# Kernel tuning notes

Hardware: AMD Instinct MI355X
Metric: run time of the kernel (lower is better)

## Reference

```python
import jax, jax.numpy as jnp
import numpy as np

GAMMA = 0.7
WALK_LEN = 3
TAU = 1.0
N_FILTERS = 8


def _row_norm(A):
    return A / jnp.clip(jnp.sum(A, axis=-1, keepdims=True), 1e-12, None)


def _motif_channel(A, idx, Wadj, gates):
    # A: [n,n]; idx: [I,k] int node indices; Wadj: [F,k,k]; gates: [L]
    n = A.shape[0]
    I, k = idx.shape
    F = Wadj.shape[0]
    # learnable filter adjacency: softplus, symmetrize, zero diagonal, row-normalize
    S = jax.nn.softplus(Wadj)
    S = 0.5 * (S + jnp.swapaxes(S, -1, -2)) * (1.0 - jnp.eye(k, dtype=A.dtype))
    Sf = _row_norm(S)                                  # [F,k,k]
    # per-instance induced subgraph transition matrices
    As = A[idx[:, :, None], idx[:, None, :]]           # [I,k,k]
    Tm = _row_norm(As)                                 # [I,k,k]
    # batched Kronecker product: Km[i,f,a*k+b,c*k+d] = Tm[i,a,c]*Sf[f,b,d]
    Km = (Tm[:, None, :, None, :, None] * Sf[None, :, None, :, None, :]).reshape(I, F, k * k, k * k)
    gp = jax.nn.softplus(gates)                        # [L] length gates
    M = Km
    acc = (GAMMA * gp[0]) * jnp.trace(M, axis1=-2, axis2=-1)   # [I,F]
    for p in range(2, WALK_LEN + 1):
        M = M @ Km
        acc = acc + (GAMMA ** p * gp[p - 1]) * jnp.trace(M, axis1=-2, axis2=-1)
    sims = acc                                         # [I,F] RWK similarities
    alphas = jax.nn.softmax(sims / max(1e-06, TAU), axis=-1)
    contrib = (alphas * sims) / float(k)               # [I,F]
    upd = jnp.broadcast_to(contrib[:, None, :], (I, k, F)).reshape(I * k, F)
    return jnp.zeros((n, F), A.dtype).at[idx.reshape(-1)].add(upd)


def _layer(A, tri_idx, cyc_idx, H, Wt, Wc, g, lng, lnb, w1, b1, w2, b2):
    Phi = jnp.concatenate([_motif_channel(A, tri_idx, Wt, g),
                           _motif_channel(A, cyc_idx, Wc, g),
                           H], axis=1)                 # [n, in_ch]
    mu = jnp.mean(Phi, axis=-1, keepdims=True)
    var = jnp.var(Phi, axis=-1, keepdims=True)
    X = (Phi - mu) / jnp.sqrt(var + 1e-5) * lng + lnb  # LayerNorm
    return jax.nn.gelu(X @ w1 + b1, approximate=False) @ w2 + b2  # dropout = identity (eval)


def _templates():
    tri = np.zeros((3, 3), np.float32)
    for u, v in [(0, 1), (1, 2), (0, 2)]:
        tri[u, v] = tri[v, u] = 1.0
    cyc = np.zeros((4, 4), np.float32)
    for u, v in [(0, 1), (1, 2), (2, 3), (3, 0)]:
        cyc[u, v] = cyc[v, u] = 1.0
    return tri, cyc


def setup_inputs() -> dict:
    key = jax.random.key(0)
    ks = jax.random.split(key, 16)
    n, D, HID = 4096, 128, 128
    A = (jax.random.uniform(ks[0], (n, n)) < 0.01).astype(jnp.float32)
    A = 0.5 * (A + A.T)
    A = A * (1.0 - jnp.eye(n, dtype=jnp.float32))
    tri_idx = jax.random.randint(ks[1], (30000, 3), 0, n, dtype=jnp.int32)
    cyc_idx = jax.random.randint(ks[2], (15000, 4), 0, n, dtype=jnp.int32)
    tri_t, cyc_t = _templates()
    def w_adj(k, tmpl):
        return jnp.asarray(tmpl)[None] + 0.05 * jax.random.normal(k, (N_FILTERS,) + tmpl.shape, dtype=jnp.float32)
    in0, in1 = 17, 145
    inp = {"A_full": A, "tri_idx": tri_idx, "cyc_idx": cyc_idx,
           "W_tri_0": w_adj(ks[3], tri_t), "W_cyc_0": w_adj(ks[4], cyc_t),
           "gates_0": jnp.zeros((WALK_LEN,), jnp.float32),
           "lng_0": jnp.ones((in0,), jnp.float32), "lnb_0": jnp.zeros((in0,), jnp.float32),
           "w1_0": 0.05 * jax.random.normal(ks[5], (in0, HID), jnp.float32), "b1_0": jnp.zeros((HID,), jnp.float32),
           "w2_0": 0.05 * jax.random.normal(ks[6], (HID, D), jnp.float32), "b2_0": jnp.zeros((D,), jnp.float32),
           "W_tri_1": w_adj(ks[7], tri_t), "W_cyc_1": w_adj(ks[8], cyc_t),
           "gates_1": jnp.zeros((WALK_LEN,), jnp.float32),
           "lng_1": jnp.ones((in1,), jnp.float32), "lnb_1": jnp.zeros((in1,), jnp.float32),
           "w1_1": 0.05 * jax.random.normal(ks[9], (in1, HID), jnp.float32), "b1_1": jnp.zeros((HID,), jnp.float32),
           "w2_1": 0.05 * jax.random.normal(ks[10], (HID, D), jnp.float32), "b2_1": jnp.zeros((D,), jnp.float32)}
    return inp


def reference(A_full, tri_idx, cyc_idx,
              W_tri_0, W_cyc_0, gates_0, lng_0, lnb_0, w1_0, b1_0, w2_0, b2_0,
              W_tri_1, W_cyc_1, gates_1, lng_1, lnb_1, w1_1, b1_1, w2_1, b2_1):
    # base channel (use_base=True): node degree from dense adjacency
    H = jnp.sum(A_full, axis=-1, keepdims=True)        # [n,1]
    Z = _layer(A_full, tri_idx, cyc_idx, H, W_tri_0, W_cyc_0, gates_0, lng_0, lnb_0, w1_0, b1_0, w2_0, b2_0)
    H = jnp.concatenate([Z, H], axis=1)                # residual_cat: [n,129]
    Z = _layer(A_full, tri_idx, cyc_idx, H, W_tri_1, W_cyc_1, gates_1, lng_1, lnb_1, w1_1, b1_1, w2_1, b2_1)
    H = jnp.concatenate([Z, H], axis=1)                # [n,257]
    return H
```

## Files before the change

kernel.cpp:

```cpp
#include <hip/hip_runtime.h>
#include <math.h>
#include <stdint.h>

#define GAMMA 0.7f
#define CAP 96

typedef __attribute__((ext_vector_type(8))) short short8v;
typedef __attribute__((ext_vector_type(4))) float f32x4;

__device__ __forceinline__ float sp_dev(float x) {
    return fmaxf(x, 0.0f) + log1pf(expf(-fabsf(x)));
}
__device__ __forceinline__ float gelu_exact(float x) {
    return 0.5f * x * (1.0f + erff(x * 0.70710678118654752f));
}
__device__ __forceinline__ uint16_t f2bf(float x) {
    union { float f; uint32_t u; } c; c.f = x;
    uint32_t u = c.u + 0x7FFFu + ((c.u >> 16) & 1u);
    return (uint16_t)(u >> 16);
}

__global__ void prep_kernel(const float* __restrict__ Wt0, const float* __restrict__ Wc0,
                            const float* __restrict__ g0,
                            const float* __restrict__ Wt1, const float* __restrict__ Wc1,
                            const float* __restrict__ g1,
                            const float* __restrict__ w1_0, const float* __restrict__ w2_0,
                            const float* __restrict__ w1_1, const float* __restrict__ w2_1,
                            float* __restrict__ dcoef,
                            uint16_t* __restrict__ Wb10, uint16_t* __restrict__ Wb20,
                            uint16_t* __restrict__ Wb11, uint16_t* __restrict__ Wb21,
                            int* __restrict__ cursor, int ncur) {
    int tid = threadIdx.x;
    int gtid = blockIdx.x * blockDim.x + tid;
    int stride = gridDim.x * blockDim.x;

    for (int i = gtid; i < ncur; i += stride) cursor[i] = 0;

    if (blockIdx.x == 0 && tid < 32) {
        int L = tid >> 4, m = (tid >> 3) & 1, f = tid & 7;
        int k = m ? 4 : 3;
        const float* W = L ? (m ? Wc1 : Wt1) : (m ? Wc0 : Wt0);
        const float* g = L ? g1 : g0;
        float S[4][4], Y[4][4];
        for (int a = 0; a < k; a++)
            for (int b = 0; b < k; b++)
                S[a][b] = sp_dev(W[(f * k + a) * k + b]);
        for (int a = 0; a < k; a++)
            for (int b = 0; b < k; b++)
                Y[a][b] = (a == b) ? 0.0f : 0.5f * (S[a][b] + S[b][a]);
        for (int a = 0; a < k; a++) {
            float rs = 0.0f;
            for (int b = 0; b < k; b++) rs += Y[a][b];
            rs = fmaxf(rs, 1e-12f);
            for (int b = 0; b < k; b++) Y[a][b] /= rs;
        }
        float t1 = 0, t2 = 0, t3 = 0;
        for (int a = 0; a < k; a++) t1 += Y[a][a];
        for (int a = 0; a < k; a++)
            for (int b = 0; b < k; b++) t2 += Y[a][b] * Y[b][a];
        for (int a = 0; a < k; a++)
            for (int b = 0; b < k; b++)
                for (int c = 0; c < k; c++) t3 += Y[a][b] * Y[b][c] * Y[c][a];
        float* d = dcoef + ((L * 2 + m) * 8 + f) * 3;
        d[0] = GAMMA * sp_dev(g[0]) * t1;
        d[1] = GAMMA * GAMMA * sp_dev(g[1]) * t2;
        d[2] = GAMMA * GAMMA * GAMMA * sp_dev(g[2]) * t3;
    }
    for (int idx = gtid; idx < 57344; idx += stride) {
        if (idx < 4096) {
            int c = idx >> 5, k = idx & 31;
            Wb10[idx] = (k < 17) ? f2bf(w1_0[k * 128 + c]) : 0;
        } else if (idx < 20480) {
            int e = idx - 4096; int c = e >> 7, k = e & 127;
            Wb20[e] = f2bf(w2_0[k * 128 + c]);
        } else if (idx < 40960) {
            int e = idx - 20480; int c = e / 160, k = e % 160;
            Wb11[e] = (k < 145) ? f2bf(w1_1[k * 128 + c]) : 0;
        } else {
            int e = idx - 40960; int c = e >> 7, k = e & 127;
            Wb21[e] = f2bf(w2_1[k * 128 + c]);
        }
    }
}

__global__ void rowsum_kernel(const float* __restrict__ A, int n,
                              float* __restrict__ H0, float* __restrict__ out) {
    int row = blockIdx.x;
    const float4* Arow = (const float4*)(A + (size_t)row * n);
    int n4 = n >> 2;
    float s = 0.0f;
    for (int i = threadIdx.x; i < n4; i += blockDim.x) {
        float4 v = Arow[i];
        s += v.x + v.y + v.z + v.w;
    }
    __shared__ float red[4];
    for (int off = 32; off > 0; off >>= 1) s += __shfl_down(s, off);
    if ((threadIdx.x & 63) == 0) red[threadIdx.x >> 6] = s;
    __syncthreads();
    if (threadIdx.x == 0) {
        float t = red[0] + red[1] + red[2] + red[3];
        H0[row] = t;
        out[(size_t)row * 257 + 256] = t;
    }
}

template <int K>
__device__ __forceinline__ void contrib_body(
    const float* __restrict__ A, int n, const int* __restrict__ idx, int I, int i,
    const float (*dc)[8][3], float* __restrict__ cont,
    int* __restrict__ cursor, int* __restrict__ slotbuf) {
    int nodes[K];
#pragma unroll
    for (int j = 0; j < K; j++) nodes[j] = idx[i * K + j];

    float Tm[K][K];
#pragma unroll
    for (int a = 0; a < K; a++) {
        float rs = 0.0f;
#pragma unroll
        for (int b = 0; b < K; b++) {
            float v = A[(size_t)nodes[a] * n + nodes[b]];
            Tm[a][b] = v; rs += v;
        }
        rs = fmaxf(rs, 1e-12f);
        float inv = 1.0f / rs;
#pragma unroll
        for (int b = 0; b < K; b++) Tm[a][b] *= inv;
    }
    float t1 = 0, t2 = 0, t3 = 0;
#pragma unroll
    for (int a = 0; a < K; a++) t1 += Tm[a][a];
#pragma unroll
    for (int a = 0; a < K; a++)
#pragma unroll
        for (int b = 0; b < K; b++) t2 += Tm[a][b] * Tm[b][a];
#pragma unroll
    for (int a = 0; a < K; a++)
#pragma unroll
        for (int b = 0; b < K; b++) {
            float ab = Tm[a][b];
#pragma unroll
            for (int c = 0; c < K; c++) t3 += ab * Tm[b][c] * Tm[c][a];
        }
#pragma unroll
    for (int L = 0; L < 2; L++) {
        float sims[8], mx = -1e30f;
#pragma unroll
        for (int f = 0; f < 8; f++) {
            sims[f] = dc[L][f][0] * t1 + dc[L][f][1] * t2 + dc[L][f][2] * t3;
            mx = fmaxf(mx, sims[f]);
        }
        float es[8], se = 0.0f;
#pragma unroll
        for (int f = 0; f < 8; f++) { es[f] = expf(sims[f] - mx); se += es[f]; }
        float inv = 1.0f / se;
        float* cp = cont + ((size_t)L * I + i) * 8;
#pragma unroll
        for (int f = 0; f < 8; f++) cp[f] = es[f] * inv * sims[f] * (1.0f / (float)K);
    }
#pragma unroll
    for (int j = 0; j < K; j++) {
        int v = nodes[j];
        int pos = atomicAdd(&cursor[v], 1);
        if (pos < CAP) slotbuf[(size_t)v * CAP + pos] = i;
    }
}

__global__ void contrib_fused_kernel(const float* __restrict__ A, int n,
                                     const int* __restrict__ tri, int Itri,
                                     const int* __restrict__ cyc, int Icyc, int B3,
                                     const float* __restrict__ dcoef,
                                     float* __restrict__ tri_c, float* __restrict__ cyc_c,
                                     int* __restrict__ cursor, int* __restrict__ slotbuf) {
    __shared__ float dc[2][8][3];
    int tid = threadIdx.x;
    bool isTri = (int)blockIdx.x < B3;
    const float* dcL0 = dcoef + (isTri ? 0 : 24);
    const float* dcL1 = dcoef + (isTri ? 48 : 72);
    if (tid < 24) dc[0][tid / 3][tid % 3] = dcL0[tid];
    else if (tid < 48) { int t = tid - 24; dc[1][t / 3][t % 3] = dcL1[t]; }
    __syncthreads();

    if (isTri) {
        int i = blockIdx.x * 256 + tid;
        if (i < Itri)
            contrib_body<3>(A, n, tri, Itri, i, dc, tri_c, cursor, slotbuf);
    } else {
        int i = (blockIdx.x - B3) * 256 + tid;
        if (i < Icyc)
            contrib_body<4>(A, n, cyc, Icyc, i, dc, cyc_c, cursor + n,
                            slotbuf + (size_t)n * CAP);
    }
}

__global__ __launch_bounds__(512) void mega_kernel(
    const float* __restrict__ tri_c, int Itri,
    const float* __restrict__ cyc_c, int Icyc,
    const int* __restrict__ cursor, const int* __restrict__ slotbuf,
    const float* __restrict__ H0,
    const float* __restrict__ lng0, const float* __restrict__ lnb0,
    const uint16_t* __restrict__ Wb10, const float* __restrict__ b1_0,
    const uint16_t* __restrict__ Wb20, const float* __restrict__ b2_0,
    const float* __restrict__ lng1, const float* __restrict__ lnb1,
    const uint16_t* __restrict__ Wb11, const float* __restrict__ b1_1,
    const uint16_t* __restrict__ Wb21, const float* __restrict__ b2_1,
    float* __restrict__ out, int n) {
    __shared__ uint16_t Xs[16][168];
    __shared__ uint16_t Hs[16][136];
    __shared__ float    Zs[16][129];
    __shared__ float    phi0[16][17];
    __shared__ float    f1[16][16];
    __shared__ float    h0s[16];

    int tid = threadIdx.x;
    int v0 = blockIdx.x * 16;
    int wave = tid >> 6;
    int lane = tid & 63;
    int lr = lane & 15, lg = lane >> 4;

    {
        int r = tid >> 5;
        int combo = tid & 31;
        int m = combo >> 4, L = (combo >> 3) & 1, f = combo & 7;
        int v = v0 + r;
        int cnt = cursor[m * n + v];
        cnt = cnt < CAP ? cnt : CAP;
        const int* bucket = slotbuf + ((size_t)(m * n + v)) * CAP;
        const float* c = m ? cyc_c : tri_c;
        int I = m ? Icyc : Itri;
        float sum = 0.0f;
        for (int j = 0; j < cnt; j++) {
            int i = bucket[j];
            sum += c[((size_t)L * I + i) * 8 + f];
        }
        if (L == 0) phi0[r][m * 8 + f] = sum;
        else        f1[r][m * 8 + f] = sum;
        if (combo == 0) { float h = H0[v]; phi0[r][16] = h; h0s[r] = h; }
    }
    __syncthreads();

    {
        int r = tid >> 5;
        int j = tid & 31;
        float x = (j < 17) ? phi0[r][j] : 0.0f;
        float s1 = x, s2 = x * x;
        for (int o = 16; o > 0; o >>= 1) { s1 += __shfl_xor(s1, o); s2 += __shfl_xor(s2, o); }
        float mu = s1 / 17.0f;
        float rstd = rsqrtf(s2 / 17.0f - mu * mu + 1e-5f);
        Xs[r][j] = (j < 17) ? f2bf((x - mu) * rstd * lng0[j] + lnb0[j]) : (uint16_t)0;
    }
    __syncthreads();

    {
        int col = wave * 16 + lr;
        f32x4 acc = {0.f, 0.f, 0.f, 0.f};
        short8v a = *(const short8v*)&Xs[lr][lg * 8];
        short8v b = *(const short8v*)(Wb10 + (size_t)col * 32 + lg * 8);
        acc = __builtin_amdgcn_mfma_f32_16x16x32_bf16(a, b, acc, 0, 0, 0);
        float bias = b1_0[col];
#pragma unroll
        for (int i = 0; i < 4; i++)
            Hs[lg * 4 + i][col] = f2bf(gelu_exact(acc[i] + bias));
    }
    __syncthreads();

    {
        int col = wave * 16 + lr;
        f32x4 acc = {0.f, 0.f, 0.f, 0.f};
#pragma unroll
        for (int ks = 0; ks < 4; ks++) {
            short8v a = *(const short8v*)&Hs[lr][ks * 32 + lg * 8];
            short8v b = *(const short8v*)(Wb20 + (size_t)col * 128 + ks * 32 + lg * 8);
            acc = __builtin_amdgcn_mfma_f32_16x16x32_bf16(a, b, acc, 0, 0, 0);
        }
        float bias = b2_0[col];
#pragma unroll
        for (int i = 0; i < 4; i++) {
            int row = lg * 4 + i;
            float val = acc[i] + bias;
            out[(size_t)(v0 + row) * 257 + 128 + col] = val;
            Zs[row][col] = val;
        }
    }
    __syncthreads();

    {
        int rr = tid >> 5;
        int t = tid & 31;
        float ph[5];
        float s1 = 0.0f, s2 = 0.0f;
#pragma unroll
        for (int s = 0; s < 5; s++) {
            int j = t + 32 * s;
            float x = 0.0f;
            if (j < 16) x = f1[rr][j];
            else if (j < 144) x = Zs[rr][j - 16];
            else if (j == 144) x = h0s[rr];
            ph[s] = x;
            if (j < 145) { s1 += x; s2 += x * x; }
        }
        for (int o = 16; o > 0; o >>= 1) { s1 += __shfl_xor(s1, o); s2 += __shfl_xor(s2, o); }
        float mu = s1 / 145.0f;
        float rstd = rsqrtf(s2 / 145.0f - mu * mu + 1e-5f);
#pragma unroll
        for (int s = 0; s < 5; s++) {
            int j = t + 32 * s;
            Xs[rr][j] = (j < 145) ? f2bf((ph[s] - mu) * rstd * lng1[j] + lnb1[j]) : (uint16_t)0;
        }
    }
    __syncthreads();

    {
        int col = wave * 16 + lr;
        f32x4 acc = {0.f, 0.f, 0.f, 0.f};
#pragma unroll
        for (int ks = 0; ks < 5; ks++) {
            short8v a = *(const short8v*)&Xs[lr][ks * 32 + lg * 8];
            short8v b = *(const short8v*)(Wb11 + (size_t)col * 160 + ks * 32 + lg * 8);
            acc = __builtin_amdgcn_mfma_f32_16x16x32_bf16(a, b, acc, 0, 0, 0);
        }
        float bias = b1_1[col];
#pragma unroll
        for (int i = 0; i < 4; i++)
            Hs[lg * 4 + i][col] = f2bf(gelu_exact(acc[i] + bias));
    }
    __syncthreads();

    {
        int col = wave * 16 + lr;
        f32x4 acc = {0.f, 0.f, 0.f, 0.f};
#pragma unroll
        for (int ks = 0; ks < 4; ks++) {
            short8v a = *(const short8v*)&Hs[lr][ks * 32 + lg * 8];
            short8v b = *(const short8v*)(Wb21 + (size_t)col * 128 + ks * 32 + lg * 8);
            acc = __builtin_amdgcn_mfma_f32_16x16x32_bf16(a, b, acc, 0, 0, 0);
        }
        float bias = b2_1[col];
#pragma unroll
        for (int i = 0; i < 4; i++) {
            int row = lg * 4 + i;
            out[(size_t)(v0 + row) * 257 + col] = acc[i] + bias;
        }
    }
}

extern "C" void kernel_launch(void* const* d_in, const int* in_sizes, int n_in,
                              void* d_out, int out_size, void* d_ws, size_t ws_size,
                              hipStream_t stream) {
    const float* A    = (const float*)d_in[0];
    const int*   tri  = (const int*)d_in[1];
    const int*   cyc  = (const int*)d_in[2];
    const float* Wt0  = (const float*)d_in[3];
    const float* Wc0  = (const float*)d_in[4];
    const float* g0   = (const float*)d_in[5];
    const float* lng0 = (const float*)d_in[6];
    const float* lnb0 = (const float*)d_in[7];
    const float* w1_0 = (const float*)d_in[8];
    const float* b1_0 = (const float*)d_in[9];
    const float* w2_0 = (const float*)d_in[10];
    const float* b2_0 = (const float*)d_in[11];
    const float* Wt1  = (const float*)d_in[12];
    const float* Wc1  = (const float*)d_in[13];
    const float* g1   = (const float*)d_in[14];
    const float* lng1 = (const float*)d_in[15];
    const float* lnb1 = (const float*)d_in[16];
    const float* w1_1 = (const float*)d_in[17];
    const float* b1_1 = (const float*)d_in[18];
    const float* w2_1 = (const float*)d_in[19];
    const float* b2_1 = (const float*)d_in[20];

    int n    = out_size / 257;
    int Itri = in_sizes[1] / 3;
    int Icyc = in_sizes[2] / 4;

    float* ws    = (float*)d_ws;
    float* dcoef = ws;
    float* H0    = ws + 128;
    float* tri_c = H0 + n;
    float* cyc_c = tri_c + (size_t)2 * Itri * 8;
    int*   cursor  = (int*)(cyc_c + (size_t)2 * Icyc * 8);
    int*   slotbuf = cursor + (size_t)2 * n;
    uint16_t* Wb10 = (uint16_t*)(slotbuf + (size_t)2 * n * CAP);
    uint16_t* Wb20 = Wb10 + 128 * 32;
    uint16_t* Wb11 = Wb20 + 128 * 128;
    uint16_t* Wb21 = Wb11 + 128 * 160;
    float* out = (float*)d_out;

    prep_kernel<<<64, 256, 0, stream>>>(Wt0, Wc0, g0, Wt1, Wc1, g1,
                                        w1_0, w2_0, w1_1, w2_1,
                                        dcoef, Wb10, Wb20, Wb11, Wb21,
                                        cursor, 2 * n);

    rowsum_kernel<<<n, 256, 0, stream>>>(A, n, H0, out);

    int B3 = (Itri + 255) / 256;
    int B4 = (Icyc + 255) / 256;
    contrib_fused_kernel<<<B3 + B4, 256, 0, stream>>>(
        A, n, tri, Itri, cyc, Icyc, B3, dcoef, tri_c, cyc_c, cursor, slotbuf);

    mega_kernel<<<n / 16, 512, 0, stream>>>(
        tri_c, Itri, cyc_c, Icyc, cursor, slotbuf, H0,
        lng0, lnb0, Wb10, b1_0, Wb20, b2_0,
        lng1, lnb1, Wb11, b1_1, Wb21, b2_1, out, n);
}
```

Before: 77.05 us.

## Fuse all stages into one kernel with per-block instance scanning

Replaces the four-kernel pipeline (prep, rowsum, contrib, mega) with a single kernel per 16-node tile. Each block recomputes the filter coefficients, sums its own adjacency rows, scans every triangle and cycle instance to queue those touching its nodes, recomputes their similarities and accumulates them with shared-memory atomics, then reads weights directly from fp32 with on-the-fly bf16 conversion. This removes three launches and the global slot buckets and cursor atomics. In exchange every block rereads the whole instance list and recomputes contributions for shared instances, and the MLP weight fragments are converted redundantly in every block.

Result: slower. 90.93 us (+18.0%).

```diff
diff --git a/kernel.cpp b/kernel.cpp
--- a/kernel.cpp
+++ b/kernel.cpp
@@ -3,7 +3,8 @@
 #include <stdint.h>
 
 #define GAMMA 0.7f
-#define CAP 96
+#define QCAP 4608
+#define NT 1024
 
 typedef __attribute__((ext_vector_type(8))) short short8v;
 typedef __attribute__((ext_vector_type(4))) float f32x4;
@@ -20,23 +21,49 @@
     return (uint16_t)(u >> 16);
 }
 
-__global__ void prep_kernel(const float* __restrict__ Wt0, const float* __restrict__ Wc0,
-                            const float* __restrict__ g0,
-                            const float* __restrict__ Wt1, const float* __restrict__ Wc1,
-                            const float* __restrict__ g1,
-                            const float* __restrict__ w1_0, const float* __restrict__ w2_0,
-                            const float* __restrict__ w1_1, const float* __restrict__ w2_1,
-                            float* __restrict__ dcoef,
-                            uint16_t* __restrict__ Wb10, uint16_t* __restrict__ Wb20,
-                            uint16_t* __restrict__ Wb11, uint16_t* __restrict__ Wb21,
-                            int* __restrict__ cursor, int ncur) {
-    int tid = threadIdx.x;
-    int gtid = blockIdx.x * blockDim.x + tid;
-    int stride = gridDim.x * blockDim.x;
-
-    for (int i = gtid; i < ncur; i += stride) cursor[i] = 0;
-
-    if (blockIdx.x == 0 && tid < 32) {
+__device__ __forceinline__ short8v wfrag(const float* __restrict__ W, int col,
+                                         int k0, int kmax) {
+    short8v r;
+#pragma unroll
+    for (int j = 0; j < 8; j++) {
+        int k = k0 + j;
+        float v = (k < kmax) ? W[(size_t)k * 128 + col] : 0.0f;
+        r[j] = (short)f2bf(v);
+    }
+    return r;
+}
+
+__global__ __launch_bounds__(NT) void uber_kernel(
+    const float* __restrict__ A, const int* __restrict__ tri, const int* __restrict__ cyc,
+    const float* __restrict__ Wt0, const float* __restrict__ Wc0, const float* __restrict__ g0,
+    const float* __restrict__ lng0, const float* __restrict__ lnb0,
+    const float* __restrict__ w1_0, const float* __restrict__ b1_0,
+    const float* __restrict__ w2_0, const float* __restrict__ b2_0,
+    const float* __restrict__ Wt1, const float* __restrict__ Wc1, const float* __restrict__ g1,
+    const float* __restrict__ lng1, const float* __restrict__ lnb1,
+    const float* __restrict__ w1_1, const float* __restrict__ b1_1,
+    const float* __restrict__ w2_1, const float* __restrict__ b2_1,
+    float* __restrict__ out, int n, int Itri, int Icyc) {
+
+    __shared__ __align__(16) char upool[QCAP * 4];
+    int* queue = (int*)upool;
+    uint16_t (*Xs)[168] = (uint16_t(*)[168])upool;
+    uint16_t (*Hs)[136] = (uint16_t(*)[136])(upool + 5376);
+    float    (*Zs)[132] = (float(*)[132])(upool + 9728);
+    __shared__ float dcs[2][2][8][3];
+    __shared__ float phiL0[16][16];
+    __shared__ float phiL1[16][16];
+    __shared__ float h0s[16];
+    __shared__ int qcnt;
+
+    const int tid  = threadIdx.x;
+    const int v0   = blockIdx.x * 16;
+    const int wave = tid >> 6;
+    const int lane = tid & 63;
+
+    if (tid < 256) { ((float*)phiL0)[tid] = 0.0f; ((float*)phiL1)[tid] = 0.0f; }
+    if (tid == 0) qcnt = 0;
+    if (tid < 32) {
         int L = tid >> 4, m = (tid >> 3) & 1, f = tid & 7;
         int k = m ? 4 : 3;
         const float* W = L ? (m ? Wc1 : Wt1) : (m ? Wc0 : Wt0);
@@ -61,188 +88,142 @@
         for (int a = 0; a < k; a++)
             for (int b = 0; b < k; b++)
                 for (int c = 0; c < k; c++) t3 += Y[a][b] * Y[b][c] * Y[c][a];
-        float* d = dcoef + ((L * 2 + m) * 8 + f) * 3;
-        d[0] = GAMMA * sp_dev(g[0]) * t1;
-        d[1] = GAMMA * GAMMA * sp_dev(g[1]) * t2;
-        d[2] = GAMMA * GAMMA * GAMMA * sp_dev(g[2]) * t3;
-    }
-    for (int idx = gtid; idx < 57344; idx += stride) {
-        if (idx < 4096) {
-            int c = idx >> 5, k = idx & 31;
-            Wb10[idx] = (k < 17) ? f2bf(w1_0[k * 128 + c]) : 0;
-        } else if (idx < 20480) {
-            int e = idx - 4096; int c = e >> 7, k = e & 127;
-            Wb20[e] = f2bf(w2_0[k * 128 + c]);
-        } else if (idx < 40960) {
-            int e = idx - 20480; int c = e / 160, k = e % 160;
-            Wb11[e] = (k < 145) ? f2bf(w1_1[k * 128 + c]) : 0;
-        } else {
-            int e = idx - 40960; int c = e >> 7, k = e & 127;
-            Wb21[e] = f2bf(w2_1[k * 128 + c]);
-        }
-    }
-}
-
-__global__ void rowsum_kernel(const float* __restrict__ A, int n,
-                              float* __restrict__ H0, float* __restrict__ out) {
-    int row = blockIdx.x;
-    const float4* Arow = (const float4*)(A + (size_t)row * n);
-    int n4 = n >> 2;
-    float s = 0.0f;
-    for (int i = threadIdx.x; i < n4; i += blockDim.x) {
-        float4 v = Arow[i];
-        s += v.x + v.y + v.z + v.w;
-    }
-    __shared__ float red[4];
-    for (int off = 32; off > 0; off >>= 1) s += __shfl_down(s, off);
-    if ((threadIdx.x & 63) == 0) red[threadIdx.x >> 6] = s;
-    __syncthreads();
-    if (threadIdx.x == 0) {
-        float t = red[0] + red[1] + red[2] + red[3];
-        H0[row] = t;
-        out[(size_t)row * 257 + 256] = t;
-    }
-}
-
-template <int K>
-__device__ __forceinline__ void contrib_body(
-    const float* __restrict__ A, int n, const int* __restrict__ idx, int I, int i,
-    const float (*dc)[8][3], float* __restrict__ cont,
-    int* __restrict__ cursor, int* __restrict__ slotbuf) {
-    int nodes[K];
-#pragma unroll
-    for (int j = 0; j < K; j++) nodes[j] = idx[i * K + j];
-
-    float Tm[K][K];
-#pragma unroll
-    for (int a = 0; a < K; a++) {
-        float rs = 0.0f;
-#pragma unroll
-        for (int b = 0; b < K; b++) {
-            float v = A[(size_t)nodes[a] * n + nodes[b]];
-            Tm[a][b] = v; rs += v;
-        }
-        rs = fmaxf(rs, 1e-12f);
-        float inv = 1.0f / rs;
-#pragma unroll
-        for (int b = 0; b < K; b++) Tm[a][b] *= inv;
-    }
-    float t1 = 0, t2 = 0, t3 = 0;
-#pragma unroll
-    for (int a = 0; a < K; a++) t1 += Tm[a][a];
-#pragma unroll
-    for (int a = 0; a < K; a++)
-#pragma unroll
-        for (int b = 0; b < K; b++) t2 += Tm[a][b] * Tm[b][a];
-#pragma unroll
-    for (int a = 0; a < K; a++)
-#pragma unroll
-        for (int b = 0; b < K; b++) {
-            float ab = Tm[a][b];
-#pragma unroll
-            for (int c = 0; c < K; c++) t3 += ab * Tm[b][c] * Tm[c][a];
-        }
-#pragma unroll
-    for (int L = 0; L < 2; L++) {
-        float sims[8], mx = -1e30f;
-#pragma unroll
-        for (int f = 0; f < 8; f++) {
-            sims[f] = dc[L][f][0] * t1 + dc[L][f][1] * t2 + dc[L][f][2] * t3;
-            mx = fmaxf(mx, sims[f]);
-        }
-        float es[8], se = 0.0f;
-#pragma unroll
-        for (int f = 0; f < 8; f++) { es[f] = expf(sims[f] - mx); se += es[f]; }
-        float inv = 1.0f / se;
-        float* cp = cont + ((size_t)L * I + i) * 8;
-#pragma unroll
-        for (int f = 0; f < 8; f++) cp[f] = es[f] * inv * sims[f] * (1.0f / (float)K);
-    }
-#pragma unroll
-    for (int j = 0; j < K; j++) {
-        int v = nodes[j];
-        int pos = atomicAdd(&cursor[v], 1);
-        if (pos < CAP) slotbuf[(size_t)v * CAP + pos] = i;
-    }
-}
-
-__global__ void contrib_fused_kernel(const float* __restrict__ A, int n,
-                                     const int* __restrict__ tri, int Itri,
-                                     const int* __restrict__ cyc, int Icyc, int B3,
-                                     const float* __restrict__ dcoef,
-                                     float* __restrict__ tri_c, float* __restrict__ cyc_c,
-                                     int* __restrict__ cursor, int* __restrict__ slotbuf) {
-    __shared__ float dc[2][8][3];
-    int tid = threadIdx.x;
-    bool isTri = (int)blockIdx.x < B3;
-    const float* dcL0 = dcoef + (isTri ? 0 : 24);
-    const float* dcL1 = dcoef + (isTri ? 48 : 72);
-    if (tid < 24) dc[0][tid / 3][tid % 3] = dcL0[tid];
-    else if (tid < 48) { int t = tid - 24; dc[1][t / 3][t % 3] = dcL1[t]; }
-    __syncthreads();
-
-    if (isTri) {
-        int i = blockIdx.x * 256 + tid;
-        if (i < Itri)
-            contrib_body<3>(A, n, tri, Itri, i, dc, tri_c, cursor, slotbuf);
-    } else {
-        int i = (blockIdx.x - B3) * 256 + tid;
-        if (i < Icyc)
-            contrib_body<4>(A, n, cyc, Icyc, i, dc, cyc_c, cursor + n,
-                            slotbuf + (size_t)n * CAP);
-    }
-}
-
-__global__ __launch_bounds__(512) void mega_kernel(
-    const float* __restrict__ tri_c, int Itri,
-    const float* __restrict__ cyc_c, int Icyc,
-    const int* __restrict__ cursor, const int* __restrict__ slotbuf,
-    const float* __restrict__ H0,
-    const float* __restrict__ lng0, const float* __restrict__ lnb0,
-    const uint16_t* __restrict__ Wb10, const float* __restrict__ b1_0,
-    const uint16_t* __restrict__ Wb20, const float* __restrict__ b2_0,
-    const float* __restrict__ lng1, const float* __restrict__ lnb1,
-    const uint16_t* __restrict__ Wb11, const float* __restrict__ b1_1,
-    const uint16_t* __restrict__ Wb21, const float* __restrict__ b2_1,
-    float* __restrict__ out, int n) {
-    __shared__ uint16_t Xs[16][168];
-    __shared__ uint16_t Hs[16][136];
-    __shared__ float    Zs[16][129];
-    __shared__ float    phi0[16][17];
-    __shared__ float    f1[16][16];
-    __shared__ float    h0s[16];
-
-    int tid = threadIdx.x;
-    int v0 = blockIdx.x * 16;
-    int wave = tid >> 6;
-    int lane = tid & 63;
-    int lr = lane & 15, lg = lane >> 4;
+        dcs[m][L][f][0] = GAMMA * sp_dev(g[0]) * t1;
+        dcs[m][L][f][1] = GAMMA * GAMMA * sp_dev(g[1]) * t2;
+        dcs[m][L][f][2] = GAMMA * GAMMA * GAMMA * sp_dev(g[2]) * t3;
+    }
 
     {
-        int r = tid >> 5;
-        int combo = tid & 31;
-        int m = combo >> 4, L = (combo >> 3) & 1, f = combo & 7;
-        int v = v0 + r;
-        int cnt = cursor[m * n + v];
-        cnt = cnt < CAP ? cnt : CAP;
-        const int* bucket = slotbuf + ((size_t)(m * n + v)) * CAP;
-        const float* c = m ? cyc_c : tri_c;
-        int I = m ? Icyc : Itri;
-        float sum = 0.0f;
-        for (int j = 0; j < cnt; j++) {
-            int i = bucket[j];
-            sum += c[((size_t)L * I + i) * 8 + f];
-        }
-        if (L == 0) phi0[r][m * 8 + f] = sum;
-        else        f1[r][m * 8 + f] = sum;
-        if (combo == 0) { float h = H0[v]; phi0[r][16] = h; h0s[r] = h; }
+        int rr = wave;
+        const float4* Ar = (const float4*)(A + (size_t)(v0 + rr) * n);
+        int n4 = n >> 2;
+        float s0 = 0, s1 = 0, s2 = 0, s3 = 0;
+        for (int i = lane; i < n4; i += 256) {
+            float4 a = Ar[i], b = Ar[i + 64], c = Ar[i + 128], d = Ar[i + 192];
+            s0 += a.x + a.y + a.z + a.w;
+            s1 += b.x + b.y + b.z + b.w;
+            s2 += c.x + c.y + c.z + c.w;
+            s3 += d.x + d.y + d.z + d.w;
+        }
+        float s = (s0 + s1) + (s2 + s3);
+        for (int o = 32; o > 0; o >>= 1) s += __shfl_down(s, o);
+        if (lane == 0) {
+            h0s[rr] = s;
+            out[(size_t)(v0 + rr) * 257 + 256] = s;
+        }
     }
     __syncthreads();
 
     {
+        int tot = Itri + Icyc;
+        for (int base = 0; base < tot; base += NT) {
+            int inst = base + tid;
+            if (inst >= tot) break;
+            int hit = 0;
+            if (inst < Itri) {
+                const int* p = tri + inst * 3;
+#pragma unroll
+                for (int j = 0; j < 3; j++) hit |= ((unsigned)(p[j] - v0) < 16u);
+            } else {
+                const int* p = cyc + (size_t)(inst - Itri) * 4;
+#pragma unroll
+                for (int j = 0; j < 4; j++) hit |= ((unsigned)(p[j] - v0) < 16u);
+            }
+            if (hit) {
+                int q = atomicAdd(&qcnt, 1);
+                if (q < QCAP) queue[q] = inst;
+            }
+        }
+    }
+    __syncthreads();
+
+    {
+        int qn = qcnt < QCAP ? qcnt : QCAP;
+        for (int qi = tid; qi < qn; qi += NT) {
+            int inst = queue[qi];
+            bool isTri = inst < Itri;
+            int m = isTri ? 0 : 1;
+            float kinv = isTri ? (1.0f / 3.0f) : 0.25f;
+            int nd[4];
+            if (isTri) {
+                const int* p = tri + inst * 3;
+                nd[0] = p[0]; nd[1] = p[1]; nd[2] = p[2]; nd[3] = 0;
+            } else {
+                const int* p = cyc + (size_t)(inst - Itri) * 4;
+                nd[0] = p[0]; nd[1] = p[1]; nd[2] = p[2]; nd[3] = p[3];
+            }
+            float M[4][4];
+#pragma unroll
+            for (int a = 0; a < 4; a++) {
+                float rs = 0.0f;
+#pragma unroll
+                for (int b = 0; b < 4; b++) {
+                    float v;
+                    if (isTri)
+                        v = (a < 3 && b < 3) ? A[(size_t)nd[a] * n + nd[b]]
+                                             : ((a == 3 && b == 3) ? 1.0f : 0.0f);
+                    else
+                        v = A[(size_t)nd[a] * n + nd[b]];
+                    M[a][b] = v; rs += v;
+                }
+                rs = fmaxf(rs, 1e-12f);
+                float inv = 1.0f / rs;
+#pragma unroll
+                for (int b = 0; b < 4; b++) M[a][b] *= inv;
+            }
+            float t1 = M[0][0] + M[1][1] + M[2][2] + M[3][3];
+            float t2 = 0, t3 = 0;
+#pragma unroll
+            for (int a = 0; a < 4; a++)
+#pragma unroll
+                for (int b = 0; b < 4; b++) {
+                    float ab = M[a][b];
+                    t2 += ab * M[b][a];
+                    float a3 = 0;
+#pragma unroll
+                    for (int c = 0; c < 4; c++) a3 += M[b][c] * M[c][a];
+                    t3 += ab * a3;
+                }
+            if (isTri) { t1 -= 1.0f; t2 -= 1.0f; t3 -= 1.0f; }
+
+            float cn[2][8];
+#pragma unroll
+            for (int L = 0; L < 2; L++) {
+                float sims[8], mx = -1e30f;
+#pragma unroll
+                for (int f = 0; f < 8; f++) {
+                    sims[f] = dcs[m][L][f][0] * t1 + dcs[m][L][f][1] * t2 +
+                              dcs[m][L][f][2] * t3;
+                    mx = fmaxf(mx, sims[f]);
+                }
+                float se = 0;
+#pragma unroll
+                for (int f = 0; f < 8; f++) { float e = expf(sims[f] - mx); cn[L][f] = e; se += e; }
+                float si = 1.0f / se;
+#pragma unroll
+                for (int f = 0; f < 8; f++) cn[L][f] = cn[L][f] * si * sims[f] * kinv;
+            }
+            int K = isTri ? 3 : 4;
+#pragma unroll
+            for (int j = 0; j < 4; j++) {
+                if (j >= K) break;
+                int r = nd[j] - v0;
+                if ((unsigned)r < 16u) {
+#pragma unroll
+                    for (int f = 0; f < 8; f++) {
+                        atomicAdd(&phiL0[r][m * 8 + f], cn[0][f]);
+                        atomicAdd(&phiL1[r][m * 8 + f], cn[1][f]);
+                    }
+                }
+            }
+        }
+    }
+    __syncthreads();
+
+    if (tid < 512) {
         int r = tid >> 5;
         int j = tid & 31;
-        float x = (j < 17) ? phi0[r][j] : 0.0f;
+        float x = (j < 16) ? phiL0[r][j] : (j == 16 ? h0s[r] : 0.0f);
         float s1 = x, s2 = x * x;
         for (int o = 16; o > 0; o >>= 1) { s1 += __shfl_xor(s1, o); s2 += __shfl_xor(s2, o); }
         float mu = s1 / 17.0f;
@@ -251,11 +232,12 @@
     }
     __syncthreads();
 
-    {
-        int col = wave * 16 + lr;
+    if (tid < 512) {
+        int w8 = tid >> 6, lr = lane & 15, lg = lane >> 4;
+        int col = w8 * 16 + lr;
         f32x4 acc = {0.f, 0.f, 0.f, 0.f};
         short8v a = *(const short8v*)&Xs[lr][lg * 8];
-        short8v b = *(const short8v*)(Wb10 + (size_t)col * 32 + lg * 8);
+        short8v b = wfrag(w1_0, col, lg * 8, 17);
         acc = __builtin_amdgcn_mfma_f32_16x16x32_bf16(a, b, acc, 0, 0, 0);
         float bias = b1_0[col];
 #pragma unroll
@@ -264,13 +246,14 @@
     }
     __syncthreads();
 
-    {
-        int col = wave * 16 + lr;
+    if (tid < 512) {
+        int w8 = tid >> 6, lr = lane & 15, lg = lane >> 4;
+        int col = w8 * 16 + lr;
         f32x4 acc = {0.f, 0.f, 0.f, 0.f};
 #pragma unroll
         for (int ks = 0; ks < 4; ks++) {
             short8v a = *(const short8v*)&Hs[lr][ks * 32 + lg * 8];
-            short8v b = *(const short8v*)(Wb20 + (size_t)col * 128 + ks * 32 + lg * 8);
+            short8v b = wfrag(w2_0, col, ks * 32 + lg * 8, 128);
             acc = __builtin_amdgcn_mfma_f32_16x16x32_bf16(a, b, acc, 0, 0, 0);
         }
         float bias = b2_0[col];
@@ -284,7 +267,7 @@
     }
     __syncthreads();
 
-    {
+    if (tid < 512) {
         int rr = tid >> 5;
         int t = tid & 31;
         float ph[5];
@@ -293,7 +276,7 @@
         for (int s = 0; s < 5; s++) {
             int j = t + 32 * s;
             float x = 0.0f;
-            if (j < 16) x = f1[rr][j];
+            if (j < 16) x = phiL1[rr][j];
             else if (j < 144) x = Zs[rr][j - 16];
             else if (j == 144) x = h0s[rr];
             ph[s] = x;
@@ -305,18 +288,20 @@
 #pragma unroll
         for (int s = 0; s < 5; s++) {
             int j = t + 32 * s;
-            Xs[rr][j] = (j < 145) ? f2bf((ph[s] - mu) * rstd * lng1[j] + lnb1[j]) : (uint16_t)0;
-        }
-    }
-    __syncthreads();
-
-    {
-        int col = wave * 16 + lr;
+            Xs[rr][j] = (j < 145) ? f2bf((ph[s] - mu) * rstd * lng1[j] + lnb1[j])
+                                  : (uint16_t)0;
+        }
+    }
+    __syncthreads();
+
+    if (tid < 512) {
+        int w8 = tid >> 6, lr = lane & 15, lg = lane >> 4;
+        int col = w8 * 16 + lr;
         f32x4 acc = {0.f, 0.f, 0.f, 0.f};
 #pragma unroll
         for (int ks = 0; ks < 5; ks++) {
             short8v a = *(const short8v*)&Xs[lr][ks * 32 + lg * 8];
-            short8v b = *(const short8v*)(Wb11 + (size_t)col * 160 + ks * 32 + lg * 8);
+            short8v b = wfrag(w1_1, col, ks * 32 + lg * 8, 145);
             acc = __builtin_amdgcn_mfma_f32_16x16x32_bf16(a, b, acc, 0, 0, 0);
         }
         float bias = b1_1[col];
@@ -326,13 +311,14 @@
     }
     __syncthreads();
 
-    {
-        int col = wave * 16 + lr;
+    if (tid < 512) {
+        int w8 = tid >> 6, lr = lane & 15, lg = lane >> 4;
+        int col = w8 * 16 + lr;
         f32x4 acc = {0.f, 0.f, 0.f, 0.f};
 #pragma unroll
         for (int ks = 0; ks < 4; ks++) {
             short8v a = *(const short8v*)&Hs[lr][ks * 32 + lg * 8];
-            short8v b = *(const short8v*)(Wb21 + (size_t)col * 128 + ks * 32 + lg * 8);
+            short8v b = wfrag(w2_1, col, ks * 32 + lg * 8, 128);
             acc = __builtin_amdgcn_mfma_f32_16x16x32_bf16(a, b, acc, 0, 0, 0);
         }
         float bias = b2_1[col];
@@ -350,56 +336,20 @@
     const float* A    = (const float*)d_in[0];
     const int*   tri  = (const int*)d_in[1];
     const int*   cyc  = (const int*)d_in[2];
-    const float* Wt0  = (const float*)d_in[3];
-    const float* Wc0  = (const float*)d_in[4];
-    const float* g0   = (const float*)d_in[5];
-    const float* lng0 = (const float*)d_in[6];
-    const float* lnb0 = (const float*)d_in[7];
-    const float* w1_0 = (const float*)d_in[8];
-    const float* b1_0 = (const float*)d_in[9];
-    const float* w2_0 = (const float*)d_in[10];
-    const float* b2_0 = (const float*)d_in[11];
-    const float* Wt1  = (const float*)d_in[12];
-    const float* Wc1  = (const float*)d_in[13];
-    const float* g1   = (const float*)d_in[14];
-    const float* lng1 = (const float*)d_in[15];
-    const float* lnb1 = (const float*)d_in[16];
-    const float* w1_1 = (const float*)d_in[17];
-    const float* b1_1 = (const float*)d_in[18];
-    const float* w2_1 = (const float*)d_in[19];
-    const float* b2_1 = (const float*)d_in[20];
 
     int n    = out_size / 257;
     int Itri = in_sizes[1] / 3;
     int Icyc = in_sizes[2] / 4;
 
-    float* ws    = (float*)d_ws;
-    float* dcoef = ws;
-    float* H0    = ws + 128;
-    float* tri_c = H0 + n;
-    float* cyc_c = tri_c + (size_t)2 * Itri * 8;
-    int*   cursor  = (int*)(cyc_c + (size_t)2 * Icyc * 8);
-    int*   slotbuf = cursor + (size_t)2 * n;
-    uint16_t* Wb10 = (uint16_t*)(slotbuf + (size_t)2 * n * CAP);
-    uint16_t* Wb20 = Wb10 + 128 * 32;
-    uint16_t* Wb11 = Wb20 + 128 * 128;
-    uint16_t* Wb21 = Wb11 + 128 * 160;
-    float* out = (float*)d_out;
-
-    prep_kernel<<<64, 256, 0, stream>>>(Wt0, Wc0, g0, Wt1, Wc1, g1,
-                                        w1_0, w2_0, w1_1, w2_1,
-                                        dcoef, Wb10, Wb20, Wb11, Wb21,
-                                        cursor, 2 * n);
-
-    rowsum_kernel<<<n, 256, 0, stream>>>(A, n, H0, out);
-
-    int B3 = (Itri + 255) / 256;
-    int B4 = (Icyc + 255) / 256;
-    contrib_fused_kernel<<<B3 + B4, 256, 0, stream>>>(
-        A, n, tri, Itri, cyc, Icyc, B3, dcoef, tri_c, cyc_c, cursor, slotbuf);
-
-    mega_kernel<<<n / 16, 512, 0, stream>>>(
-        tri_c, Itri, cyc_c, Icyc, cursor, slotbuf, H0,
-        lng0, lnb0, Wb10, b1_0, Wb20, b2_0,
-        lng1, lnb1, Wb11, b1_1, Wb21, b2_1, out, n);
-}
+    uber_kernel<<<n / 16, NT, 0, stream>>>(
+        A, tri, cyc,
+        (const float*)d_in[3], (const float*)d_in[4], (const float*)d_in[5],
+        (const float*)d_in[6], (const float*)d_in[7],
+        (const float*)d_in[8], (const float*)d_in[9],
+        (const float*)d_in[10], (const float*)d_in[11],
+        (const float*)d_in[12], (const float*)d_in[13], (const float*)d_in[14],
+        (const float*)d_in[15], (const float*)d_in[16],
+        (const float*)d_in[17], (const float*)d_in[18],
+        (const float*)d_in[19], (const float*)d_in[20],
+        (float*)d_out, n, Itri, Icyc);
+}
```
